# Optimization experiments

Hardware: AMD Instinct MI355X
Metric: run time of the kernel (lower is better)

The kernel has to match this reference:

```python
import jax, jax.numpy as jnp
import numpy as np

N, K, D = 262144, 256, 128
SCALE = 0.1
LOG2PI = float(np.log(2.0 * np.pi))


def setup_inputs() -> dict:
    key = jax.random.key(0)
    k_in, k_mu, k_ls, k_noise = jax.random.split(key, 4)
    return {
        "input": jax.random.normal(k_in, (N, D), dtype=jnp.float32),
        "means": jax.random.normal(k_mu, (K, D), dtype=jnp.float32),
        "log_stds": jax.random.normal(k_ls, (K, D), dtype=jnp.float32) * 0.5,
        "weights": jnp.ones((K,), dtype=jnp.float32),
        "noise": jax.random.normal(k_noise, (N, D), dtype=jnp.float32),
    }


def _gmm_forward(x, means, log_stds, weights, noise):
    d = x.shape[-1]
    # Diagonal-Gaussian log-prob per component, via GEMM decomposition:
    inv_var = jnp.exp(-2.0 * log_stds)                      # [K, D]
    quad = (
        (x * x) @ inv_var.T                                  # [N, K]
        - 2.0 * (x @ (means * inv_var).T)                    # [N, K]
        + jnp.sum(means * means * inv_var, axis=-1)          # [K]
    )
    log_p_x_z = -0.5 * (quad + d * LOG2PI) - jnp.sum(log_stds, axis=-1)  # [N, K]
    log_p_z = jax.nn.log_softmax(weights)                    # [K]
    joint = log_p_x_z + log_p_z                              # [N, K]
    p_z_x = jax.nn.softmax(joint + 1e-8, axis=-1)            # [N, K]
    idxs = jnp.argmax(p_z_x, axis=-1)                        # [N]
    Q = jnp.mean(jax.lax.stop_gradient(p_z_x) * joint)       # scalar
    # Resample from the selected component (noise replaces randn_like)
    resampled_x = means[idxs] + jnp.exp(log_stds[idxs]) * noise * SCALE
    return resampled_x, idxs, Q


def reference(input, means, log_stds, weights, noise):
    return _gmm_forward(input, means, log_stds, weights, noise)
```

## Files before the change

kernel.cpp:

```cpp
#include <hip/hip_runtime.h>
#include <math.h>

#define N_ROWS 262144
#define K_COMP 256
#define D_DIM  128
#define BN 64
#define KIN 256

typedef _Float16 half8v __attribute__((ext_vector_type(8)));
typedef _Float16 half4v __attribute__((ext_vector_type(4)));
typedef float    f32x4  __attribute__((ext_vector_type(4)));

static __device__ __constant__ float kLOG2PI = 1.8378770664093453f;

__global__ __launch_bounds__(128) void gmm_prep(
    const float* __restrict__ means, const float* __restrict__ log_stds,
    const float* __restrict__ weights,
    _Float16* __restrict__ Bhi, _Float16* __restrict__ Blo,
    float* __restrict__ sigma, float* __restrict__ ck, double* __restrict__ wsq)
{
    int k = blockIdx.x;
    int d = threadIdx.x;
    float ls = log_stds[k * D_DIM + d];
    float mu = means[k * D_DIM + d];
    float iv = expf(-2.0f * ls);
    float m2 = -2.0f * mu * iv;
    sigma[k * D_DIM + d] = expf(ls);

    {
        int c = k >> 4;
        #pragma unroll
        for (int t = 0; t < 2; ++t) {
            int kin = t * 128 + d;
            float val = t ? m2 : iv;
            int s = kin >> 5;
            int l = ((kin >> 3) & 3) * 16 + (k & 15);
            int j = kin & 7;
            int lin = ((c * 8 + s) * 64 + l) * 8 + j;
            _Float16 hi = (_Float16)val;
            Bhi[lin] = hi;
            Blo[lin] = (_Float16)(val - (float)hi);
        }
    }

    float c = mu * mu * iv;
    float s = ls;
    float w1 = weights[d], w2 = weights[d + 128];
    float wm = fmaxf(w1, w2);

    __shared__ float red[8];
    int lane = d & 63, wv = d >> 6;
    #pragma unroll
    for (int o = 32; o > 0; o >>= 1) {
        c += __shfl_down(c, o, 64);
        s += __shfl_down(s, o, 64);
        wm = fmaxf(wm, __shfl_down(wm, o, 64));
    }
    if (lane == 0) { red[wv] = c; red[2 + wv] = s; red[4 + wv] = wm; }
    __syncthreads();
    float csum = red[0] + red[1];
    float ssum = red[2] + red[3];
    float wmax = fmaxf(red[4], red[5]);
    float we = expf(w1 - wmax) + expf(w2 - wmax);
    #pragma unroll
    for (int o = 32; o > 0; o >>= 1) we += __shfl_down(we, o, 64);
    if (lane == 0) red[6 + wv] = we;
    __syncthreads();
    if (d == 0) {
        float wsum = red[6] + red[7];
        float lw = weights[k] - (wmax + logf(wsum));
        ck[k] = -0.5f * (csum + (float)D_DIM * kLOG2PI) - ssum + lw;
        if (k == 0) *wsq = 0.0;
    }
}

__global__ __launch_bounds__(256, 3) void gmm_main(
    const float* __restrict__ x, const float* __restrict__ noise,
    const float* __restrict__ means, const float* __restrict__ sigma,
    const _Float16* __restrict__ Bhi, const _Float16* __restrict__ Blo,
    const float* __restrict__ ck,
    float* __restrict__ out_x, float* __restrict__ out_idx, double* __restrict__ wsq)
{
    __shared__ char  sA[2][BN * 256];
    __shared__ float sCk[K_COMP];
    __shared__ float sMax[BN][4];
    __shared__ int   sAm [BN][4];
    __shared__ float sEs [BN][4];
    __shared__ float sQs [BN][4];
    __shared__ int   sIdx[BN];

    const int tid = threadIdx.x;
    const int w   = tid >> 6;
    const int l   = tid & 63;
    const int lm  = l & 15;
    const int lh  = l >> 4;
    const long n0 = (long)blockIdx.x * BN;

    sCk[tid] = ck[tid];

    float4 xv[8];
    {
        const float4* xg = (const float4*)(x + (size_t)n0 * D_DIM);
        #pragma unroll
        for (int it = 0; it < 8; ++it) xv[it] = xg[it * 256 + tid];
    }

    #pragma unroll
    for (int it = 0; it < 8; ++it) {
        int g = it * 256 + tid;
        int row = g >> 5, d4 = g & 31;
        float xe[4] = {xv[it].x, xv[it].y, xv[it].z, xv[it].w};
        half4v h, lo;
        #pragma unroll
        for (int cc = 0; cc < 4; ++cc) {
            float vv = xe[cc] * xe[cc];
            _Float16 a = (_Float16)vv;
            h[cc] = a; lo[cc] = (_Float16)(vv - (float)a);
        }
        unsigned off = ((unsigned)(row * 256 + d4 * 8)) ^ ((unsigned)(row & 7) << 4);
        *(half4v*)(sA[0] + off) = h;
        *(half4v*)(sA[1] + off) = lo;
    }
    __syncthreads();

    f32x4 acc[4][4];
    #pragma unroll
    for (int rf = 0; rf < 4; ++rf)
        #pragma unroll
        for (int cf = 0; cf < 4; ++cf)
            acc[rf][cf] = (f32x4){0.0f, 0.0f, 0.0f, 0.0f};

    const half8v* Bh = (const half8v*)Bhi;
    const half8v* Bl = (const half8v*)Blo;

    #pragma unroll 2
    for (int s = 0; s < 4; ++s) {
        half8v ah[4], al[4], bh4[4], bl4[4];
        #pragma unroll
        for (int rf = 0; rf < 4; ++rf) {
            int row = rf * 16 + lm;
            unsigned off = ((unsigned)(row * 256 + s * 64 + lh * 16))
                         ^ ((unsigned)(row & 7) << 4);
            ah[rf] = *(const half8v*)(sA[0] + off);
            al[rf] = *(const half8v*)(sA[1] + off);
        }
        #pragma unroll
        for (int cf = 0; cf < 4; ++cf) {
            int bidx = ((w * 4 + cf) * 8 + s) * 64 + l;
            bh4[cf] = Bh[bidx];
            bl4[cf] = Bl[bidx];
        }
        #pragma unroll
        for (int rf = 0; rf < 4; ++rf)
            #pragma unroll
            for (int cf = 0; cf < 4; ++cf) {
                acc[rf][cf] = __builtin_amdgcn_mfma_f32_16x16x32_f16(ah[rf], bh4[cf], acc[rf][cf], 0, 0, 0);
                acc[rf][cf] = __builtin_amdgcn_mfma_f32_16x16x32_f16(ah[rf], bl4[cf], acc[rf][cf], 0, 0, 0);
                acc[rf][cf] = __builtin_amdgcn_mfma_f32_16x16x32_f16(al[rf], bh4[cf], acc[rf][cf], 0, 0, 0);
            }
    }
    __syncthreads();

    #pragma unroll
    for (int it = 0; it < 8; ++it) {
        int g = it * 256 + tid;
        int row = g >> 5, d4 = g & 31;
        float xe[4] = {xv[it].x, xv[it].y, xv[it].z, xv[it].w};
        half4v h, lo;
        #pragma unroll
        for (int cc = 0; cc < 4; ++cc) {
            float v = xe[cc];
            _Float16 a = (_Float16)v;
            h[cc] = a; lo[cc] = (_Float16)(v - (float)a);
        }
        unsigned off = ((unsigned)(row * 256 + d4 * 8)) ^ ((unsigned)(row & 7) << 4);
        *(half4v*)(sA[0] + off) = h;
        *(half4v*)(sA[1] + off) = lo;
    }
    __syncthreads();

    #pragma unroll 2
    for (int s = 4; s < 8; ++s) {
        half8v ah[4], al[4], bh4[4], bl4[4];
        #pragma unroll
        for (int rf = 0; rf < 4; ++rf) {
            int row = rf * 16 + lm;
            unsigned off = ((unsigned)(row * 256 + (s - 4) * 64 + lh * 16))
                         ^ ((unsigned)(row & 7) << 4);
            ah[rf] = *(const half8v*)(sA[0] + off);
            al[rf] = *(const half8v*)(sA[1] + off);
        }
        #pragma unroll
        for (int cf = 0; cf < 4; ++cf) {
            int bidx = ((w * 4 + cf) * 8 + s) * 64 + l;
            bh4[cf] = Bh[bidx];
            bl4[cf] = Bl[bidx];
        }
        #pragma unroll
        for (int rf = 0; rf < 4; ++rf)
            #pragma unroll
            for (int cf = 0; cf < 4; ++cf) {
                acc[rf][cf] = __builtin_amdgcn_mfma_f32_16x16x32_f16(ah[rf], bh4[cf], acc[rf][cf], 0, 0, 0);
                acc[rf][cf] = __builtin_amdgcn_mfma_f32_16x16x32_f16(ah[rf], bl4[cf], acc[rf][cf], 0, 0, 0);
                acc[rf][cf] = __builtin_amdgcn_mfma_f32_16x16x32_f16(al[rf], bh4[cf], acc[rf][cf], 0, 0, 0);
            }
    }

    float ckv[4];
    #pragma unroll
    for (int cf = 0; cf < 4; ++cf) ckv[cf] = sCk[w * 64 + cf * 16 + lm];

    #pragma unroll
    for (int rf = 0; rf < 4; ++rf) {
        #pragma unroll
        for (int reg = 0; reg < 4; ++reg) {
            int row = rf * 16 + lh * 4 + reg;
            float jv[4];
            float m = -INFINITY; int am = 0;
            #pragma unroll
            for (int cf = 0; cf < 4; ++cf) {
                float v = fmaf(-0.5f, acc[rf][cf][reg], ckv[cf]);
                jv[cf] = v;
                int col = w * 64 + cf * 16 + lm;
                if (v > m) { m = v; am = col; }
            }
            #pragma unroll
            for (int o = 1; o < 16; o <<= 1) {
                float om = __shfl_xor(m, o, 16);
                int   oa = __shfl_xor(am, o, 16);
                if (om > m || (om == m && oa < am)) { m = om; am = oa; }
            }
            float es = 0.0f, qs = 0.0f;
            #pragma unroll
            for (int cf = 0; cf < 4; ++cf) {
                float e = expf(jv[cf] - m);
                es += e; qs = fmaf(e, jv[cf], qs);
            }
            #pragma unroll
            for (int o = 1; o < 16; o <<= 1) {
                es += __shfl_xor(es, o, 16);
                qs += __shfl_xor(qs, o, 16);
            }
            if (lm == 0) {
                sMax[row][w] = m; sAm[row][w] = am;
                sEs [row][w] = es; sQs[row][w] = qs;
            }
        }
    }
    __syncthreads();

    if (tid < BN) {
        const int row = tid;
        float m = sMax[row][0]; int am = sAm[row][0];
        float es = sEs[row][0], qs = sQs[row][0];
        #pragma unroll
        for (int w2 = 1; w2 < 4; ++w2) {
            float mw = sMax[row][w2];
            if (mw > m) {
                float f = expf(m - mw);
                es = es * f + sEs[row][w2];
                qs = qs * f + sQs[row][w2];
                m = mw; am = sAm[row][w2];
            } else {
                float f = expf(mw - m);
                es += sEs[row][w2] * f;
                qs += sQs[row][w2] * f;
            }
        }
        sIdx[row] = am;
        float q = qs / es;
        #pragma unroll
        for (int o = 1; o < 64; o <<= 1) q += __shfl_xor(q, o, 64);
        if (tid == 0) atomicAdd(wsq, (double)q);
    }
    __syncthreads();

    const int wv = tid >> 6, lane = tid & 63;
    #pragma unroll 4
    for (int r16 = 0; r16 < 16; ++r16) {
        const int row = wv * 16 + r16;
        const int idx = sIdx[row];
        const long n = n0 + row;
        float2 mv = *(const float2*)&means[idx * D_DIM + lane * 2];
        float2 sv = *(const float2*)&sigma[idx * D_DIM + lane * 2];
        float2 nv = *(const float2*)&noise[n * D_DIM + lane * 2];
        float2 ov;
        ov.x = mv.x + sv.x * nv.x * 0.1f;
        ov.y = mv.y + sv.y * nv.y * 0.1f;
        *(float2*)&out_x[n * D_DIM + lane * 2] = ov;
    }
    if (tid < BN) out_idx[n0 + tid] = (float)sIdx[tid];
}

__global__ void gmm_finalize(const double* __restrict__ wsq, float* __restrict__ out_q)
{
    *out_q = (float)(*wsq * (1.0 / ((double)N_ROWS * (double)K_COMP)));
}

extern "C" void kernel_launch(void* const* d_in, const int* in_sizes, int n_in,
                              void* d_out, int out_size, void* d_ws, size_t ws_size,
                              hipStream_t stream)
{
    const float* x        = (const float*)d_in[0];
    const float* means    = (const float*)d_in[1];
    const float* log_stds = (const float*)d_in[2];
    const float* weights  = (const float*)d_in[3];
    const float* noise    = (const float*)d_in[4];

    float* out_x   = (float*)d_out;
    float* out_idx = (float*)d_out + (size_t)N_ROWS * D_DIM;
    float* out_q   = out_idx + N_ROWS;

    float*     ws    = (float*)d_ws;
    _Float16*  Bhi   = (_Float16*)ws;
    _Float16*  Blo   = (_Float16*)(ws + 32768);
    float*     sigma = ws + 65536;
    float*     ckp   = ws + 98304;
    double*    wsq   = (double*)(ws + 98560);

    hipLaunchKernelGGL(gmm_prep, dim3(K_COMP), dim3(D_DIM), 0, stream,
                       means, log_stds, weights, Bhi, Blo, sigma, ckp, wsq);
    hipLaunchKernelGGL(gmm_main, dim3(N_ROWS / BN), dim3(256), 0, stream,
                       x, noise, means, sigma, Bhi, Blo, ckp, out_x, out_idx, wsq);
    hipLaunchKernelGGL(gmm_finalize, dim3(1), dim3(1), 0, stream, wsq, out_q);
}
```

Measured before the change: 469.4 us.

## Reload x after first GEMM half, prefetch noise before reduction, use fast exp

The kernel no longer keeps the x tile in 32 registers across the first MFMA phase. It re-reads x from global memory just before the barrier for the second phase. The noise rows are prefetched into registers before the cross-wave reduction, so their latency overlaps the reduction and the resample loop does not stall on them, and that loop is fully unrolled. expf and the division are swapped for __expf and __fdividef. This aims to lower register pressure during the GEMM and hide memory latency, at the cost of a second read of x (likely an L2 hit), extra live registers for noise, and slightly less accurate exponentials.

```diff
diff --git a/kernel.cpp b/kernel.cpp
--- a/kernel.cpp
+++ b/kernel.cpp
@@ -98,18 +98,14 @@
 
     sCk[tid] = ck[tid];
 
-    float4 xv[8];
-    {
-        const float4* xg = (const float4*)(x + (size_t)n0 * D_DIM);
-        #pragma unroll
-        for (int it = 0; it < 8; ++it) xv[it] = xg[it * 256 + tid];
-    }
+    const float4* xg = (const float4*)(x + (size_t)n0 * D_DIM);
 
     #pragma unroll
     for (int it = 0; it < 8; ++it) {
         int g = it * 256 + tid;
         int row = g >> 5, d4 = g & 31;
-        float xe[4] = {xv[it].x, xv[it].y, xv[it].z, xv[it].w};
+        float4 xv = xg[g];
+        float xe[4] = {xv.x, xv.y, xv.z, xv.w};
         half4v h, lo;
         #pragma unroll
         for (int cc = 0; cc < 4; ++cc) {
@@ -159,13 +155,18 @@
                 acc[rf][cf] = __builtin_amdgcn_mfma_f32_16x16x32_f16(al[rf], bh4[cf], acc[rf][cf], 0, 0, 0);
             }
     }
+
+    float4 xv2[8];
+    #pragma unroll
+    for (int it = 0; it < 8; ++it) xv2[it] = xg[it * 256 + tid];
+
     __syncthreads();
 
     #pragma unroll
     for (int it = 0; it < 8; ++it) {
         int g = it * 256 + tid;
         int row = g >> 5, d4 = g & 31;
-        float xe[4] = {xv[it].x, xv[it].y, xv[it].z, xv[it].w};
+        float xe[4] = {xv2[it].x, xv2[it].y, xv2[it].z, xv2[it].w};
         half4v h, lo;
         #pragma unroll
         for (int cc = 0; cc < 4; ++cc) {
@@ -233,7 +234,7 @@
             float es = 0.0f, qs = 0.0f;
             #pragma unroll
             for (int cf = 0; cf < 4; ++cf) {
-                float e = expf(jv[cf] - m);
+                float e = __expf(jv[cf] - m);
                 es += e; qs = fmaf(e, jv[cf], qs);
             }
             #pragma unroll
@@ -247,6 +248,13 @@
             }
         }
     }
+
+    const int wv = tid >> 6, lane = tid & 63;
+    float2 nvv[16];
+    #pragma unroll
+    for (int r16 = 0; r16 < 16; ++r16)
+        nvv[r16] = *(const float2*)&noise[(n0 + wv * 16 + r16) * D_DIM + lane * 2];
+
     __syncthreads();
 
     if (tid < BN) {
@@ -257,36 +265,34 @@
         for (int w2 = 1; w2 < 4; ++w2) {
             float mw = sMax[row][w2];
             if (mw > m) {
-                float f = expf(m - mw);
+                float f = __expf(m - mw);
                 es = es * f + sEs[row][w2];
                 qs = qs * f + sQs[row][w2];
                 m = mw; am = sAm[row][w2];
             } else {
-                float f = expf(mw - m);
+                float f = __expf(mw - m);
                 es += sEs[row][w2] * f;
                 qs += sQs[row][w2] * f;
             }
         }
         sIdx[row] = am;
-        float q = qs / es;
+        float q = __fdividef(qs, es);
         #pragma unroll
         for (int o = 1; o < 64; o <<= 1) q += __shfl_xor(q, o, 64);
         if (tid == 0) atomicAdd(wsq, (double)q);
     }
     __syncthreads();
 
-    const int wv = tid >> 6, lane = tid & 63;
-    #pragma unroll 4
+    #pragma unroll
     for (int r16 = 0; r16 < 16; ++r16) {
         const int row = wv * 16 + r16;
         const int idx = sIdx[row];
         const long n = n0 + row;
         float2 mv = *(const float2*)&means[idx * D_DIM + lane * 2];
         float2 sv = *(const float2*)&sigma[idx * D_DIM + lane * 2];
-        float2 nv = *(const float2*)&noise[n * D_DIM + lane * 2];
         float2 ov;
-        ov.x = mv.x + sv.x * nv.x * 0.1f;
-        ov.y = mv.y + sv.y * nv.y * 0.1f;
+        ov.x = mv.x + sv.x * nvv[r16].x * 0.1f;
+        ov.y = mv.y + sv.y * nvv[r16].y * 0.1f;
         *(float2*)&out_x[n * D_DIM + lane * 2] = ov;
     }
     if (tid < BN) out_idx[n0 + tid] = (float)sIdx[tid];
```

Result: faster. 421.7 us (-10.2%).
